# Kernel tuning notes

Hardware: AMD Instinct MI355X
Metric: run time of the kernel (lower is better)

Reference implementation:

```python
import jax, jax.numpy as jnp
import numpy as np

B, T, D_IN, H, D_LIN, K = 128, 512, 102, 256, 128, 9


def _lstm_scan(xs, Wih, Whh, b):
    # xs: [T, B, D]; PyTorch gate order i, f, g, o
    Bb = xs.shape[1]
    def step(carry, x_t):
        h, c = carry
        g = x_t @ Wih.T + h @ Whh.T + b
        i, f, gg, o = jnp.split(g, 4, axis=-1)
        c = jax.nn.sigmoid(f) * c + jax.nn.sigmoid(i) * jnp.tanh(gg)
        h = jax.nn.sigmoid(o) * jnp.tanh(c)
        return (h, c), h
    init = (jnp.zeros((Bb, H), xs.dtype), jnp.zeros((Bb, H), xs.dtype))
    _, hs = jax.lax.scan(step, init, xs)
    return hs  # [T, B, H]


def _crf_nll(em, labels, mask, start_t, end_t, trans):
    # em: [B,T,K], labels: [B,T] int, mask: [B,T] bool (mask[:,0] assumed True)
    Bb = em.shape[0]
    mf = mask.astype(em.dtype)
    bidx = jnp.arange(Bb)
    # ----- numerator: score of the gold path -----
    num = start_t[labels[:, 0]] + em[bidx, 0, labels[:, 0]]
    lt = trans[labels[:, :-1], labels[:, 1:]]                       # [B,T-1]
    le = jnp.take_along_axis(em, labels[:, :, None], axis=2)[:, :, 0]  # [B,T]
    num = num + (lt * mf[:, 1:]).sum(1) + (le[:, 1:] * mf[:, 1:]).sum(1)
    last_idx = (mf.sum(1) - 1).astype(jnp.int32)
    num = num + end_t[labels[bidx, last_idx]]
    # ----- denominator: log partition via forward algorithm -----
    alpha0 = start_t[None, :] + em[:, 0]                             # [B,K]
    def step(alpha, inp):
        em_t, m_t = inp  # [B,K], [B]
        nxt = jax.nn.logsumexp(alpha[:, :, None] + trans[None] + em_t[:, None, :], axis=1)
        return jnp.where(m_t[:, None], nxt, alpha), None
    alpha, _ = jax.lax.scan(step, alpha0, (em.transpose(1, 0, 2)[1:], mask.T[1:]))
    logZ = jax.nn.logsumexp(alpha + end_t[None, :], axis=1)
    return -(num - logZ).sum()  # torchcrf reduction='sum'; model returns -crf(...)


def setup_inputs() -> dict:
    key = jax.random.key(0)
    ks = jax.random.split(key, 16)
    s = 0.05
    inp = {
        "x": jax.random.normal(ks[0], (B, T, D_IN), jnp.float32),
        "seq_len": jnp.full((B,), T, jnp.int64 if jax.config.jax_enable_x64 else jnp.int32),
        "labels": jax.random.randint(ks[1], (B, T), 0, K),
        "mask": jnp.ones((B, T), jnp.bool_),
        # forward-direction LSTM params (PyTorch layout [4H, in], [4H, H]); biases fused
        "Wih_f": jax.random.normal(ks[2], (4 * H, D_IN), jnp.float32) * s,
        "Whh_f": jax.random.normal(ks[3], (4 * H, H), jnp.float32) * s,
        "b_f": jax.random.normal(ks[4], (4 * H,), jnp.float32) * s,
        # backward-direction LSTM params
        "Wih_b": jax.random.normal(ks[5], (4 * H, D_IN), jnp.float32) * s,
        "Whh_b": jax.random.normal(ks[6], (4 * H, H), jnp.float32) * s,
        "b_b": jax.random.normal(ks[7], (4 * H,), jnp.float32) * s,
        "Wlin": jax.random.normal(ks[8], (D_LIN, 2 * H), jnp.float32) * s,
        "blin": jax.random.normal(ks[9], (D_LIN,), jnp.float32) * s,
        "Wcls": jax.random.normal(ks[10], (K, D_LIN), jnp.float32) * s,
        "bcls": jax.random.normal(ks[11], (K,), jnp.float32) * s,
        "start_t": jax.random.normal(ks[12], (K,), jnp.float32) * 0.1,
        "end_t": jax.random.normal(ks[13], (K,), jnp.float32) * 0.1,
        "trans": jax.random.normal(ks[14], (K, K), jnp.float32) * 0.1,
    }
    return inp


def reference(x, seq_len, labels, mask, Wih_f, Whh_f, b_f, Wih_b, Whh_b, b_b,
              Wlin, blin, Wcls, bcls, start_t, end_t, trans):
    # seq_len is uniformly T, so pack/pad round-trips are identity.
    xs = x.transpose(1, 0, 2)                       # [T,B,D]
    h_fwd = _lstm_scan(xs, Wih_f, Whh_f, b_f)       # [T,B,H]
    h_bwd = _lstm_scan(xs[::-1], Wih_b, Whh_b, b_b)[::-1]
    feats = jnp.concatenate([h_fwd, h_bwd], axis=-1).transpose(1, 0, 2)  # [B,T,2H]
    # dropout is identity in eval mode
    feats = jax.nn.elu(feats @ Wlin.T + blin)
    emissions = feats @ Wcls.T + bcls               # [B,T,K]
    return _crf_nll(emissions, labels, mask, start_t, end_t, trans)
```

## Files before the change

kernel.cpp:

```cpp
#include <hip/hip_runtime.h>
#include <hip/hip_bf16.h>

typedef unsigned short u16;
typedef unsigned int u32;
typedef unsigned long long u64;
typedef __attribute__((ext_vector_type(8))) short bf16x8;
typedef __attribute__((ext_vector_type(4))) float f32x4;
typedef __attribute__((ext_vector_type(4))) unsigned short u16x4;

#define MFMA_B16(a,b,c) __builtin_amdgcn_mfma_f32_16x16x32_bf16((a),(b),(c),0,0,0)

#define BB 128
#define TT 512
#define HH 256
#define DIN 102

__device__ __forceinline__ u16 f2bf(float f){
  unsigned u = __float_as_uint(f);
  u += 0x7fffu + ((u >> 16) & 1u);
  return (u16)(u >> 16);
}
__device__ __forceinline__ float bf2f(u16 v){ return __uint_as_float(((unsigned)v) << 16); }
__device__ __forceinline__ float sigm(float x){ return 1.f/(1.f + __expf(-x)); }
__device__ __forceinline__ float tanh_f(float x){ return 1.f - 2.f/(__expf(2.f*x) + 1.f); }

__global__ __launch_bounds__(256) void pack_x(const float* __restrict__ x, u16* __restrict__ xT){
  int idx = blockIdx.x*256 + threadIdx.x;
  int c = idx & 127, b = (idx >> 7) & 127, t = idx >> 14;
  float v = (c < DIN) ? x[((size_t)b*TT + t)*DIN + c] : 0.f;
  xT[idx] = f2bf(v);
}
__global__ __launch_bounds__(256) void pack_whh(const float* __restrict__ wf, const float* __restrict__ wb,
                                                u16* __restrict__ dst){
  int idx = blockIdx.x*256 + threadIdx.x;
  int d = idx >> 18; int s = idx & 0x3FFFF;
  dst[idx] = f2bf((d ? wb : wf)[s]);
}
__global__ __launch_bounds__(256) void pack_wih(const float* __restrict__ wf, const float* __restrict__ wb,
                                                u16* __restrict__ dst){
  int idx = blockIdx.x*256 + threadIdx.x;
  int d = idx >> 17; int r = (idx >> 7) & 1023; int k = idx & 127;
  float v = (k < DIN) ? (d ? wb : wf)[r*DIN + k] : 0.f;
  dst[idx] = f2bf(v);
}
__global__ __launch_bounds__(256) void pack_wlin(const float* __restrict__ w, u16* __restrict__ dst){
  int idx = blockIdx.x*256 + threadIdx.x;
  dst[idx] = f2bf(w[idx]);
}

__global__ __launch_bounds__(256, 1) void lstm_scan(
    const u16* __restrict__ xT, const u16* __restrict__ Whh,
    const u16* __restrict__ Wih, const float* __restrict__ b_f,
    const float* __restrict__ b_b, u32* __restrict__ Hst32,
    u32* __restrict__ flags)
{
  const int w  = blockIdx.x;
  const int hs = w >> 4;
  const int d  = (w >> 3) & 1;
  const int bt = w & 7;
  const int tid = threadIdx.x;
  const int wv = tid >> 6, lane = tid & 63;
  const int r16 = lane & 15, kq = lane >> 4;

  __shared__ float gacc[4][4][16][17];

  bf16x8 wfh[4][2], wfi[4];
  const float* bias = d ? b_b : b_f;
  float bias_r[4];
  #pragma unroll
  for (int g = 0; g < 4; ++g) {
    int row = g*256 + hs*16 + r16;
    const u16* ph = Whh + ((size_t)d*1024 + row)*256 + wv*64 + kq*8;
    wfh[g][0] = *(const bf16x8*)ph;
    wfh[g][1] = *(const bf16x8*)(ph + 32);
    const u16* pi = Wih + ((size_t)d*1024 + row)*128 + wv*32 + kq*8;
    wfi[g] = *(const bf16x8*)pi;
    bias_r[g] = (wv == 0) ? bias[row] : 0.f;
  }

  const int pb = tid >> 4, pj = tid & 15;
  const int btb = bt*16;
  float c_state = 0.f;

  for (int s = 0; s < TT; ++s) {
    const int t = d ? (TT-1 - s) : s;
    const int tprev = d ? (t + 1) : (t - 1);

    f32x4 acc[4];
    #pragma unroll
    for (int g = 0; g < 4; ++g) acc[g] = (f32x4){bias_r[g],bias_r[g],bias_r[g],bias_r[g]};

    const u16* xp = xT + ((size_t)t*BB + btb + r16)*128 + wv*32 + kq*8;
    bf16x8 xa = *(const bf16x8*)xp;
    #pragma unroll
    for (int g = 0; g < 4; ++g) acc[g] = MFMA_B16(xa, wfi[g], acc[g]);

    if (s > 0) {
      const u32* fb = flags + ((size_t)((d*TT + tprev)*8 + bt))*64;
      if (lane < 4) {
        while (__hip_atomic_load(&fb[(wv*4 + lane)*4], __ATOMIC_RELAXED,
                                 __HIP_MEMORY_SCOPE_AGENT) == 0u) { }
      }
      asm volatile("" ::: "memory");

      const u64* hp = (const u64*)(Hst32 +
          (((size_t)d*TT + tprev)*BB + btb + r16)*128 + wv*32 + kq*4);
      u64 q0 = __hip_atomic_load(hp + 0, __ATOMIC_RELAXED, __HIP_MEMORY_SCOPE_AGENT);
      u64 q1 = __hip_atomic_load(hp + 1, __ATOMIC_RELAXED, __HIP_MEMORY_SCOPE_AGENT);
      u64 q2 = __hip_atomic_load(hp + 8, __ATOMIC_RELAXED, __HIP_MEMORY_SCOPE_AGENT);
      u64 q3 = __hip_atomic_load(hp + 9, __ATOMIC_RELAXED, __HIP_MEMORY_SCOPE_AGENT);
      union U { u64 q[2]; bf16x8 v; } u0, u1;
      u0.q[0] = q0; u0.q[1] = q1;
      u1.q[0] = q2; u1.q[1] = q3;
      bf16x8 ha0 = u0.v, ha1 = u1.v;
      #pragma unroll
      for (int g = 0; g < 4; ++g) {
        acc[g] = MFMA_B16(ha0, wfh[g][0], acc[g]);
        acc[g] = MFMA_B16(ha1, wfh[g][1], acc[g]);
      }
    }

    #pragma unroll
    for (int g = 0; g < 4; ++g)
      #pragma unroll
      for (int rr = 0; rr < 4; ++rr)
        gacc[wv][g][kq*4 + rr][r16] = acc[g][rr];
    __syncthreads();

    float iv = 0.f, fv = 0.f, gv = 0.f, ov = 0.f;
    #pragma unroll
    for (int u = 0; u < 4; ++u) {
      iv += gacc[u][0][pb][pj];
      fv += gacc[u][1][pb][pj];
      gv += gacc[u][2][pb][pj];
      ov += gacc[u][3][pb][pj];
    }
    float ig = sigm(iv), fg = sigm(fv), gg = tanh_f(gv), og = sigm(ov);
    c_state = fg*c_state + ig*gg;
    float h = og * tanh_f(c_state);

    float hpart = __shfl_xor(h, 1, 64);
    if ((pj & 1) == 0) {
      u32 pk = (u32)f2bf(h) | ((u32)f2bf(hpart) << 16);
      size_t idx = (((size_t)d*TT + t)*BB + btb + pb)*128 + hs*8 + (pj >> 1);
      __hip_atomic_store(&Hst32[idx], pk, __ATOMIC_RELAXED, __HIP_MEMORY_SCOPE_AGENT);
    }
    asm volatile("s_waitcnt vmcnt(0)" ::: "memory");
    __syncthreads();
    if (tid == 0)
      __hip_atomic_store(&flags[((size_t)((d*TT + t)*8 + bt))*64 + hs*4], 1u,
                         __ATOMIC_RELAXED, __HIP_MEMORY_SCOPE_AGENT);
  }
}

__global__ __launch_bounds__(256) void linear_elu(
    const u16* __restrict__ Hst, const u16* __restrict__ Wlin_pk,
    const float* __restrict__ blin, u16* __restrict__ feats2)
{
  const int t = blockIdx.x;
  const int tid = threadIdx.x;
  const int wv = tid >> 6, lane = tid & 63;
  const int r16 = lane & 15, kq = lane >> 4;
  __shared__ u16 w1s[32*512];

  f32x4 acc[2][8];
  #pragma unroll
  for (int mi = 0; mi < 2; ++mi)
    #pragma unroll
    for (int nt = 0; nt < 8; ++nt) {
      float bv = blin[nt*16 + r16];
      acc[mi][nt] = (f32x4){bv,bv,bv,bv};
    }

  #pragma unroll
  for (int q = 0; q < 4; ++q) {
    __syncthreads();
    for (int i = tid; i < 2048; i += 256) {
      int rl = i >> 6, ch = i & 63;
      int dst = rl*1024 + ((ch*16) ^ ((rl & 7) << 4));
      *(bf16x8*)((char*)w1s + dst) = *(const bf16x8*)(Wlin_pk + (size_t)(q*32 + rl)*512 + ch*8);
    }
    __syncthreads();
    #pragma unroll
    for (int mi = 0; mi < 2; ++mi) {
      const int mb = (wv*2 + mi)*16;
      #pragma unroll
      for (int kc = 0; kc < 16; ++kc) {
        const int dd = kc >> 3, ki = kc & 7;
        const u16* ap = Hst + (((size_t)dd*TT + t)*BB + mb + r16)*256 + ki*32 + kq*8;
        bf16x8 a = *(const bf16x8*)ap;
        #pragma unroll
        for (int ntl = 0; ntl < 2; ++ntl) {
          int rl = ntl*16 + r16;
          int boff = kc*64 + kq*16;
          const u16* bp = (const u16*)((const char*)w1s + rl*1024 + (boff ^ ((rl & 7) << 4)));
          acc[mi][q*2 + ntl] = MFMA_B16(a, *(const bf16x8*)bp, acc[mi][q*2 + ntl]);
        }
      }
    }
  }
  #pragma unroll
  for (int mi = 0; mi < 2; ++mi) {
    const int mb = (wv*2 + mi)*16;
    #pragma unroll
    for (int nt = 0; nt < 8; ++nt) {
      u16x4 pk;
      #pragma unroll
      for (int rr = 0; rr < 4; ++rr) {
        float y = acc[mi][nt][rr];
        y = (y > 0.f) ? y : (__expf(y) - 1.f);
        pk[rr] = f2bf(y);
      }
      int n = nt*16 + r16;
      int bcol = mb + kq*4;
      *(u16x4*)(feats2 + ((size_t)t*128 + n)*BB + bcol) = pk;
    }
  }
}

__global__ __launch_bounds__(256) void cls_kernel(
    const u16* __restrict__ feats2, const float* __restrict__ Wcls,
    const float* __restrict__ bcls, float* __restrict__ em)
{
  __shared__ float w2s[9*128];
  __shared__ float b2s[9];
  const int tid = threadIdx.x;
  for (int i = tid; i < 9*128; i += 256) w2s[i] = Wcls[i];
  if (tid < 9) b2s[tid] = bcls[tid];
  __syncthreads();
  const int bb = tid & 127;
  const int t = blockIdx.x*2 + (tid >> 7);
  float accv[9];
  #pragma unroll
  for (int j = 0; j < 9; ++j) accv[j] = b2s[j];
  for (int n = 0; n < 128; ++n) {
    float y = bf2f(feats2[((size_t)t*128 + n)*BB + bb]);
    #pragma unroll
    for (int j = 0; j < 9; ++j) accv[j] = fmaf(w2s[j*128 + n], y, accv[j]);
  }
  #pragma unroll
  for (int j = 0; j < 9; ++j) em[((size_t)bb*TT + t)*9 + j] = accv[j];
}

__global__ __launch_bounds__(64) void crf_kernel(
    const float* __restrict__ em, const int* __restrict__ labels,
    const float* __restrict__ start_t, const float* __restrict__ end_t,
    const float* __restrict__ trans, float* __restrict__ vals)
{
  const int b = blockIdx.x;
  const int lane = threadIdx.x;
  __shared__ float tr_s[81];
  for (int i = lane; i < 81; i += 64) tr_s[i] = trans[i];
  __syncthreads();
  const int* lb = labels + (size_t)b*TT;
  const float* emb = em + (size_t)b*TT*9;

  float nsum = 0.f;
  for (int t = lane; t < TT; t += 64) {
    int lt = lb[t];
    float v = emb[t*9 + lt];
    v += (t == 0) ? start_t[lt] : tr_s[lb[t-1]*9 + lt];
    nsum += v;
  }
  #pragma unroll
  for (int o = 32; o > 0; o >>= 1) nsum += __shfl_down(nsum, o, 64);

  float tr_reg[9];
  #pragma unroll
  for (int i = 0; i < 9; ++i) tr_reg[i] = 0.f;
  if (lane < 9) {
    #pragma unroll
    for (int i = 0; i < 9; ++i) tr_reg[i] = tr_s[i*9 + lane];
  }
  float alpha_j = (lane < 9) ? (start_t[lane] + emb[lane]) : -1e30f;
  float a_all[9];
  #pragma unroll
  for (int i = 0; i < 9; ++i) a_all[i] = __shfl(alpha_j, i, 64);
  float em_c = (lane < 9) ? emb[9 + lane] : 0.f;
  for (int t = 1; t < TT; ++t) {
    float em_n = 0.f;
    if (t + 1 < TT && lane < 9) em_n = emb[(t+1)*9 + lane];
    float av[9];
    #pragma unroll
    for (int i = 0; i < 9; ++i) av[i] = a_all[i] + tr_reg[i];
    float m = av[0];
    #pragma unroll
    for (int i = 1; i < 9; ++i) m = fmaxf(m, av[i]);
    float ssum = 0.f;
    #pragma unroll
    for (int i = 0; i < 9; ++i) ssum += __expf(av[i] - m);
    float nxt = m + __logf(ssum) + em_c;
    #pragma unroll
    for (int i = 0; i < 9; ++i) a_all[i] = __shfl(nxt, i, 64);
    em_c = em_n;
  }
  if (lane == 0) {
    float vv[9];
    #pragma unroll
    for (int i = 0; i < 9; ++i) vv[i] = a_all[i] + end_t[i];
    float m = vv[0];
    #pragma unroll
    for (int i = 1; i < 9; ++i) m = fmaxf(m, vv[i]);
    float ssum = 0.f;
    #pragma unroll
    for (int i = 0; i < 9; ++i) ssum += __expf(vv[i] - m);
    float logZ = m + __logf(ssum);
    float num = nsum + end_t[lb[TT-1]];
    vals[b] = num - logZ;
  }
}

__global__ __launch_bounds__(128) void finalize_k(const float* __restrict__ vals, float* __restrict__ out){
  const int tid = threadIdx.x;
  float v = vals[tid];
  #pragma unroll
  for (int o = 32; o > 0; o >>= 1) v += __shfl_down(v, o, 64);
  __shared__ float sr[2];
  if ((tid & 63) == 0) sr[tid >> 6] = v;
  __syncthreads();
  if (tid == 0) out[0] = -(sr[0] + sr[1]);
}

extern "C" void kernel_launch(void* const* d_in, const int* in_sizes, int n_in,
                              void* d_out, int out_size, void* d_ws, size_t ws_size,
                              hipStream_t stream)
{
  const float* x       = (const float*)d_in[0];
  const int*   labels  = (const int*)d_in[2];
  const float* Wih_f   = (const float*)d_in[4];
  const float* Whh_f   = (const float*)d_in[5];
  const float* b_f     = (const float*)d_in[6];
  const float* Wih_b   = (const float*)d_in[7];
  const float* Whh_b   = (const float*)d_in[8];
  const float* b_b     = (const float*)d_in[9];
  const float* Wlin    = (const float*)d_in[10];
  const float* blin    = (const float*)d_in[11];
  const float* Wcls    = (const float*)d_in[12];
  const float* bcls    = (const float*)d_in[13];
  const float* start_t = (const float*)d_in[14];
  const float* end_t   = (const float*)d_in[15];
  const float* trans   = (const float*)d_in[16];

  char* p = (char*)d_ws;
  u16* xT     = (u16*)p;  p += (size_t)TT*BB*128*2;
  u16* WhhP   = (u16*)p;  p += (size_t)2*1024*256*2;
  u16* WihP   = (u16*)p;  p += (size_t)2*1024*128*2;
  u16* WlinP  = (u16*)p;  p += (size_t)128*512*2;
  u32* Hst32  = (u32*)p;  p += (size_t)2*TT*BB*128*4;
  u16* feats2 = (u16*)p;  p += (size_t)TT*128*BB*2;
  float* em   = (float*)p; p += (size_t)BB*TT*9*4;
  u32* flags  = (u32*)p;  p += (size_t)2*TT*8*64*4;
  float* vals = (float*)p; p += 128*4;

  hipMemsetAsync(flags, 0, (size_t)2*TT*8*64*4, stream);
  pack_x   <<<32768, 256, 0, stream>>>(x, xT);
  pack_whh <<<2048,  256, 0, stream>>>(Whh_f, Whh_b, WhhP);
  pack_wih <<<1024,  256, 0, stream>>>(Wih_f, Wih_b, WihP);
  pack_wlin<<<256,   256, 0, stream>>>(Wlin, WlinP);
  lstm_scan<<<256,   256, 0, stream>>>(xT, WhhP, WihP, b_f, b_b, Hst32, flags);
  linear_elu<<<512,  256, 0, stream>>>((const u16*)Hst32, WlinP, blin, feats2);
  cls_kernel<<<256,  256, 0, stream>>>(feats2, Wcls, bcls, em);
  crf_kernel<<<128,  64,  0, stream>>>(em, labels, start_t, end_t, trans, vals);
  finalize_k<<<1,    128, 0, stream>>>(vals, (float*)d_out);
}
```

Before: 1.315 ms.

## Replace flag-based LSTM step sync with NaN-sentinel polling in single-wave blocks

The recurrent LSTM kernel moves from 4-wave blocks, which split K and reduce partial gate sums through LDS with two barriers per step, to a single wave per block that holds the full K slice of the weights in registers. Cross-block dependencies no longer go through separate flag stores and spin loops. Instead, the hidden-state buffer is pre-filled with a NaN sentinel pattern and consumers reload h until no sentinel remains. This removes the flag round trip, the vmcnt wait and the LDS reduction from the serial critical path. In exchange, each block has 4x fewer threads doing 4x the MFMA work, there is an extra fill pass over the hidden-state buffer, and a real bf16 value equal to the sentinel would hang the kernel.

```diff
diff --git a/kernel.cpp b/kernel.cpp
--- a/kernel.cpp
+++ b/kernel.cpp
@@ -7,6 +7,7 @@
 typedef __attribute__((ext_vector_type(8))) short bf16x8;
 typedef __attribute__((ext_vector_type(4))) float f32x4;
 typedef __attribute__((ext_vector_type(4))) unsigned short u16x4;
+typedef __attribute__((ext_vector_type(4))) u32 u32x4;
 
 #define MFMA_B16(a,b,c) __builtin_amdgcn_mfma_f32_16x16x32_bf16((a),(b),(c),0,0,0)
 
@@ -14,6 +15,8 @@
 #define TT 512
 #define HH 256
 #define DIN 102
+
+#define SENT32 0x7FC07FC0u
 
 __device__ __forceinline__ u16 f2bf(float f){
   unsigned u = __float_as_uint(f);
@@ -47,40 +50,40 @@
   int idx = blockIdx.x*256 + threadIdx.x;
   dst[idx] = f2bf(w[idx]);
 }
-
-__global__ __launch_bounds__(256, 1) void lstm_scan(
+__global__ __launch_bounds__(256) void fill_sent(u32x4* __restrict__ p){
+  size_t i = (size_t)blockIdx.x*256 + threadIdx.x;
+  p[i] = (u32x4){SENT32, SENT32, SENT32, SENT32};
+}
+
+__global__ __launch_bounds__(64, 1) void lstm_scan(
     const u16* __restrict__ xT, const u16* __restrict__ Whh,
     const u16* __restrict__ Wih, const float* __restrict__ b_f,
-    const float* __restrict__ b_b, u32* __restrict__ Hst32,
-    u32* __restrict__ flags)
+    const float* __restrict__ b_b, u32* __restrict__ Hst32)
 {
   const int w  = blockIdx.x;
   const int hs = w >> 4;
   const int d  = (w >> 3) & 1;
   const int bt = w & 7;
-  const int tid = threadIdx.x;
-  const int wv = tid >> 6, lane = tid & 63;
+  const int lane = threadIdx.x & 63;
   const int r16 = lane & 15, kq = lane >> 4;
 
-  __shared__ float gacc[4][4][16][17];
-
-  bf16x8 wfh[4][2], wfi[4];
+  bf16x8 wfh[4][8], wfi[4][4];
+  float bias_r[4];
   const float* bias = d ? b_b : b_f;
-  float bias_r[4];
   #pragma unroll
   for (int g = 0; g < 4; ++g) {
-    int row = g*256 + hs*16 + r16;
-    const u16* ph = Whh + ((size_t)d*1024 + row)*256 + wv*64 + kq*8;
-    wfh[g][0] = *(const bf16x8*)ph;
-    wfh[g][1] = *(const bf16x8*)(ph + 32);
-    const u16* pi = Wih + ((size_t)d*1024 + row)*128 + wv*32 + kq*8;
-    wfi[g] = *(const bf16x8*)pi;
-    bias_r[g] = (wv == 0) ? bias[row] : 0.f;
-  }
-
-  const int pb = tid >> 4, pj = tid & 15;
+    const int row = g*256 + hs*16 + r16;
+    const u16* ph = Whh + ((size_t)d*1024 + row)*256 + kq*8;
+    #pragma unroll
+    for (int c = 0; c < 8; ++c) wfh[g][c] = *(const bf16x8*)(ph + c*32);
+    const u16* pi = Wih + ((size_t)d*1024 + row)*128 + kq*8;
+    #pragma unroll
+    for (int c = 0; c < 4; ++c) wfi[g][c] = *(const bf16x8*)(pi + c*32);
+    bias_r[g] = bias[row];
+  }
+
   const int btb = bt*16;
-  float c_state = 0.f;
+  f32x4 c_state = (f32x4){0.f, 0.f, 0.f, 0.f};
 
   for (int s = 0; s < TT; ++s) {
     const int t = d ? (TT-1 - s) : s;
@@ -88,68 +91,68 @@
 
     f32x4 acc[4];
     #pragma unroll
-    for (int g = 0; g < 4; ++g) acc[g] = (f32x4){bias_r[g],bias_r[g],bias_r[g],bias_r[g]};
-
-    const u16* xp = xT + ((size_t)t*BB + btb + r16)*128 + wv*32 + kq*8;
-    bf16x8 xa = *(const bf16x8*)xp;
-    #pragma unroll
-    for (int g = 0; g < 4; ++g) acc[g] = MFMA_B16(xa, wfi[g], acc[g]);
+    for (int g = 0; g < 4; ++g) acc[g] = (f32x4){bias_r[g], bias_r[g], bias_r[g], bias_r[g]};
+
+    const u16* xp = xT + ((size_t)t*BB + btb + r16)*128 + kq*8;
+    bf16x8 xa0 = *(const bf16x8*)(xp);
+    bf16x8 xa1 = *(const bf16x8*)(xp + 32);
+    bf16x8 xa2 = *(const bf16x8*)(xp + 64);
+    bf16x8 xa3 = *(const bf16x8*)(xp + 96);
+    #pragma unroll
+    for (int g = 0; g < 4; ++g) {
+      acc[g] = MFMA_B16(xa0, wfi[g][0], acc[g]);
+      acc[g] = MFMA_B16(xa1, wfi[g][1], acc[g]);
+      acc[g] = MFMA_B16(xa2, wfi[g][2], acc[g]);
+      acc[g] = MFMA_B16(xa3, wfi[g][3], acc[g]);
+    }
 
     if (s > 0) {
-      const u32* fb = flags + ((size_t)((d*TT + tprev)*8 + bt))*64;
-      if (lane < 4) {
-        while (__hip_atomic_load(&fb[(wv*4 + lane)*4], __ATOMIC_RELAXED,
-                                 __HIP_MEMORY_SCOPE_AGENT) == 0u) { }
-      }
-      asm volatile("" ::: "memory");
-
       const u64* hp = (const u64*)(Hst32 +
-          (((size_t)d*TT + tprev)*BB + btb + r16)*128 + wv*32 + kq*4);
-      u64 q0 = __hip_atomic_load(hp + 0, __ATOMIC_RELAXED, __HIP_MEMORY_SCOPE_AGENT);
-      u64 q1 = __hip_atomic_load(hp + 1, __ATOMIC_RELAXED, __HIP_MEMORY_SCOPE_AGENT);
-      u64 q2 = __hip_atomic_load(hp + 8, __ATOMIC_RELAXED, __HIP_MEMORY_SCOPE_AGENT);
-      u64 q3 = __hip_atomic_load(hp + 9, __ATOMIC_RELAXED, __HIP_MEMORY_SCOPE_AGENT);
-      union U { u64 q[2]; bf16x8 v; } u0, u1;
-      u0.q[0] = q0; u0.q[1] = q1;
-      u1.q[0] = q2; u1.q[1] = q3;
-      bf16x8 ha0 = u0.v, ha1 = u1.v;
+          (((size_t)d*TT + tprev)*BB + btb + r16)*128) + kq*2;
+      u64 q[16];
+      while (true) {
+        #pragma unroll
+        for (int c = 0; c < 8; ++c) {
+          q[2*c]   = __hip_atomic_load(hp + c*8,     __ATOMIC_RELAXED, __HIP_MEMORY_SCOPE_AGENT);
+          q[2*c+1] = __hip_atomic_load(hp + c*8 + 1, __ATOMIC_RELAXED, __HIP_MEMORY_SCOPE_AGENT);
+        }
+        u32 bad = 0u;
+        #pragma unroll
+        for (int i = 0; i < 16; ++i) {
+          bad |= (u32)(((u32)q[i]) == SENT32);
+          bad |= (u32)(((u32)(q[i] >> 32)) == SENT32);
+        }
+        if (!bad) break;
+      }
       #pragma unroll
-      for (int g = 0; g < 4; ++g) {
-        acc[g] = MFMA_B16(ha0, wfh[g][0], acc[g]);
-        acc[g] = MFMA_B16(ha1, wfh[g][1], acc[g]);
-      }
-    }
-
-    #pragma unroll
-    for (int g = 0; g < 4; ++g)
+      for (int c = 0; c < 8; ++c) {
+        union { u64 a[2]; bf16x8 v; } u;
+        u.a[0] = q[2*c]; u.a[1] = q[2*c+1];
+        #pragma unroll
+        for (int g = 0; g < 4; ++g) acc[g] = MFMA_B16(u.v, wfh[g][c], acc[g]);
+      }
+    }
+
+    float hv[4], hx[4];
+    #pragma unroll
+    for (int rr = 0; rr < 4; ++rr) {
+      float ig = sigm(acc[0][rr]);
+      float fg = sigm(acc[1][rr]);
+      float gg = tanh_f(acc[2][rr]);
+      float og = sigm(acc[3][rr]);
+      c_state[rr] = fg*c_state[rr] + ig*gg;
+      hv[rr] = og * tanh_f(c_state[rr]);
+    }
+    #pragma unroll
+    for (int rr = 0; rr < 4; ++rr) hx[rr] = __shfl_xor(hv[rr], 1, 64);
+    if ((r16 & 1) == 0) {
       #pragma unroll
-      for (int rr = 0; rr < 4; ++rr)
-        gacc[wv][g][kq*4 + rr][r16] = acc[g][rr];
-    __syncthreads();
-
-    float iv = 0.f, fv = 0.f, gv = 0.f, ov = 0.f;
-    #pragma unroll
-    for (int u = 0; u < 4; ++u) {
-      iv += gacc[u][0][pb][pj];
-      fv += gacc[u][1][pb][pj];
-      gv += gacc[u][2][pb][pj];
-      ov += gacc[u][3][pb][pj];
-    }
-    float ig = sigm(iv), fg = sigm(fv), gg = tanh_f(gv), og = sigm(ov);
-    c_state = fg*c_state + ig*gg;
-    float h = og * tanh_f(c_state);
-
-    float hpart = __shfl_xor(h, 1, 64);
-    if ((pj & 1) == 0) {
-      u32 pk = (u32)f2bf(h) | ((u32)f2bf(hpart) << 16);
-      size_t idx = (((size_t)d*TT + t)*BB + btb + pb)*128 + hs*8 + (pj >> 1);
-      __hip_atomic_store(&Hst32[idx], pk, __ATOMIC_RELAXED, __HIP_MEMORY_SCOPE_AGENT);
-    }
-    asm volatile("s_waitcnt vmcnt(0)" ::: "memory");
-    __syncthreads();
-    if (tid == 0)
-      __hip_atomic_store(&flags[((size_t)((d*TT + t)*8 + bt))*64 + hs*4], 1u,
-                         __ATOMIC_RELAXED, __HIP_MEMORY_SCOPE_AGENT);
+      for (int rr = 0; rr < 4; ++rr) {
+        u32 pk = (u32)f2bf(hv[rr]) | ((u32)f2bf(hx[rr]) << 16);
+        size_t idx = (((size_t)d*TT + t)*BB + btb + kq*4 + rr)*128 + hs*8 + (r16 >> 1);
+        __hip_atomic_store(&Hst32[idx], pk, __ATOMIC_RELAXED, __HIP_MEMORY_SCOPE_AGENT);
+      }
+    }
   }
 }
 
@@ -349,15 +352,14 @@
   u32* Hst32  = (u32*)p;  p += (size_t)2*TT*BB*128*4;
   u16* feats2 = (u16*)p;  p += (size_t)TT*128*BB*2;
   float* em   = (float*)p; p += (size_t)BB*TT*9*4;
-  u32* flags  = (u32*)p;  p += (size_t)2*TT*8*64*4;
   float* vals = (float*)p; p += 128*4;
 
-  hipMemsetAsync(flags, 0, (size_t)2*TT*8*64*4, stream);
+  fill_sent<<<16384, 256, 0, stream>>>((u32x4*)Hst32);
   pack_x   <<<32768, 256, 0, stream>>>(x, xT);
   pack_whh <<<2048,  256, 0, stream>>>(Whh_f, Whh_b, WhhP);
   pack_wih <<<1024,  256, 0, stream>>>(Wih_f, Wih_b, WihP);
   pack_wlin<<<256,   256, 0, stream>>>(Wlin, WlinP);
-  lstm_scan<<<256,   256, 0, stream>>>(xT, WhhP, WihP, b_f, b_b, Hst32, flags);
+  lstm_scan<<<256,   64,  0, stream>>>(xT, WhhP, WihP, b_f, b_b, Hst32);
   linear_elu<<<512,  256, 0, stream>>>((const u16*)Hst32, WlinP, blin, feats2);
   cls_kernel<<<256,  256, 0, stream>>>(feats2, Wcls, bcls, em);
   crf_kernel<<<128,  64,  0, stream>>>(em, labels, start_t, end_t, trans, vals);
```

Result: slower. 1.446 ms (+9.9%).
